# Kernel tuning notes

Measured on AMD Instinct MI355X. Metric: run time of the kernel, lower is better.

The kernel has to match this reference:

```python
import jax, jax.numpy as jnp
import numpy as np
import math

N_ITEMS = 200000
N_USERS = 100000
D = 128
E_II = 3200000
E_UI = 1600000


def spmm(src, dst, val, x, n_rows):
    # out[i] = sum_{e: dst[e]==i} val[e] * x[src[e]]
    return jax.ops.segment_sum(val[:, None] * x[src], dst, num_segments=n_rows)


def leaky_relu(x):
    return jnp.where(x >= 0, x, 0.2 * x)


def setup_inputs() -> dict:
    key = jax.random.key(0)
    ks = jax.random.split(key, 16)
    d = {}
    d["b"] = 2
    d["items_emb"] = jax.random.normal(ks[0], (N_ITEMS, D), dtype=jnp.float32) * 0.1
    for i, rel in enumerate(["p2p_in", "p2p_out", "e2p_in"]):
        d[f"src_{rel}"] = jax.random.randint(ks[1 + 3 * i], (E_II,), 0, N_ITEMS, dtype=jnp.int32)
        d[f"dst_{rel}"] = jax.random.randint(ks[2 + 3 * i], (E_II,), 0, N_ITEMS, dtype=jnp.int32)
        d[f"val_{rel}"] = jax.random.uniform(ks[3 + 3 * i], (E_II,), dtype=jnp.float32) / 16.0
    d["src_ui"] = jax.random.randint(ks[10], (E_UI,), 0, N_ITEMS, dtype=jnp.int32)
    d["dst_ui"] = jax.random.randint(ks[11], (E_UI,), 0, N_USERS, dtype=jnp.int32)
    d["val_ui"] = jax.random.uniform(ks[12], (E_UI,), dtype=jnp.float32) / 16.0
    s = 1.0 / math.sqrt(D)
    d["I_p2p_in"] = jax.random.normal(ks[13], (D, D), dtype=jnp.float32) * s
    d["I_p2p_out"] = jax.random.normal(ks[14], (D, D), dtype=jnp.float32) * s
    d["I_e2p_in"] = jax.random.normal(ks[15], (D, D), dtype=jnp.float32) * s
    return d


def reference(b, items_emb, src_p2p_in, dst_p2p_in, val_p2p_in,
              src_p2p_out, dst_p2p_out, val_p2p_out,
              src_e2p_in, dst_e2p_in, val_e2p_in,
              src_ui, dst_ui, val_ui,
              I_p2p_in, I_p2p_out, I_e2p_in):
    assert b == 2  # static branch, matches torch `if b == 2`
    x = items_emb
    n = x.shape[0]
    inv_sqrt_d = 1.0 / math.sqrt(x.shape[1])

    # multi-relation sparse aggregation (torch.spmm)
    nb_in = spmm(src_p2p_in, dst_p2p_in, val_p2p_in, x, n)
    nb_out = spmm(src_p2p_out, dst_p2p_out, val_p2p_out, x, n)
    nb_e2p = spmm(src_e2p_in, dst_e2p_in, val_e2p_in, x, n)

    # gated attention over relations
    h_in = leaky_relu((x * nb_in) @ I_p2p_in)
    h_out = leaky_relu((x * nb_out) @ I_p2p_out)
    h_e2p = leaky_relu((x * nb_e2p) @ I_e2p_in)
    s_in = jnp.sum(h_in, axis=1) * inv_sqrt_d
    s_out = jnp.sum(h_out, axis=1) * inv_sqrt_d
    s_e2p = jnp.sum(h_e2p, axis=1) * inv_sqrt_d
    score = jax.nn.softmax(jnp.stack((s_in, s_out, s_e2p), axis=1), axis=1)  # [n,3]
    neighbor = (nb_in * score[:, 0:1]
                + nb_out * score[:, 1:2]
                + nb_e2p * score[:, 2:3])

    # uiGNN: user embeddings from item embeddings
    u_emb = spmm(src_ui, dst_ui, val_ui, x, N_USERS)
    return (u_emb, neighbor)
```

## Files before the change

kernel.cpp:

```cpp
#include <hip/hip_runtime.h>

#define D 128
#define N_ITEMS 200000
#define N_USERS 100000
#define TI 32

#define INV_SQRT_D 0.088388347648318447f

__global__ __launch_bounds__(256) void hist_kernel(
    const int* __restrict__ dst, unsigned* __restrict__ counts, int E)
{
    int e = blockIdx.x * 256 + threadIdx.x;
    if (e < E) atomicAdd(&counts[dst[e]], 1u);
}

__global__ __launch_bounds__(256) void scan1_kernel(
    const unsigned* __restrict__ counts, unsigned* __restrict__ offsets,
    unsigned* __restrict__ blocksums, int n)
{
    __shared__ unsigned s[256];
    int tid = threadIdx.x;
    int i = blockIdx.x * 256 + tid;
    unsigned v = (i < n) ? counts[i] : 0u;
    s[tid] = v; __syncthreads();
    #pragma unroll
    for (int off = 1; off < 256; off <<= 1) {
        unsigned t = (tid >= off) ? s[tid - off] : 0u;
        __syncthreads();
        s[tid] += t;
        __syncthreads();
    }
    if (i < n) offsets[i] = s[tid] - v;
    if (tid == 255) blocksums[blockIdx.x] = s[255];
}

__global__ __launch_bounds__(1024) void scan2_kernel(
    unsigned* __restrict__ blocksums, int nb)
{
    __shared__ unsigned s[1024];
    int tid = threadIdx.x;
    unsigned v = (tid < nb) ? blocksums[tid] : 0u;
    s[tid] = v; __syncthreads();
    #pragma unroll
    for (int off = 1; off < 1024; off <<= 1) {
        unsigned t = (tid >= off) ? s[tid - off] : 0u;
        __syncthreads();
        s[tid] += t;
        __syncthreads();
    }
    if (tid < nb) blocksums[tid] = s[tid] - v;
}

__global__ __launch_bounds__(256) void scan3_kernel(
    unsigned* __restrict__ offsets, unsigned* __restrict__ cursor,
    const unsigned* __restrict__ blocksums, int n, unsigned Etot)
{
    int i = blockIdx.x * 256 + threadIdx.x;
    if (i < n) {
        unsigned o = offsets[i] + blocksums[blockIdx.x];
        offsets[i] = o;
        cursor[i] = o;
    }
    if (i == 0) offsets[n] = Etot;
}

__global__ __launch_bounds__(256) void scatter_kernel(
    const int* __restrict__ src, const int* __restrict__ dst,
    const float* __restrict__ val, unsigned* __restrict__ cursor,
    int2* __restrict__ pairs, int E)
{
    int e = blockIdx.x * 256 + threadIdx.x;
    if (e >= E) return;
    unsigned pos = atomicAdd(&cursor[dst[e]], 1u);
    pairs[pos] = make_int2(src[e], __float_as_int(val[e]));
}

__global__ __launch_bounds__(256) void gather_spmm_kernel(
    const unsigned* __restrict__ offsets, const int2* __restrict__ pairs,
    const float4* __restrict__ x4, float4* __restrict__ out4, int nrows)
{
    int row = blockIdx.x * 8 + (threadIdx.x >> 5);
    if (row >= nrows) return;
    int lane = threadIdx.x & 31;
    unsigned j = offsets[row], end = offsets[row + 1];
    float4 acc = make_float4(0.f, 0.f, 0.f, 0.f);
    for (; j + 2 <= end; j += 2) {
        int2 p0 = pairs[j];
        int2 p1 = pairs[j + 1];
        float4 a = x4[(size_t)p0.x * 32 + lane];
        float4 b = x4[(size_t)p1.x * 32 + lane];
        float v0 = __int_as_float(p0.y), v1 = __int_as_float(p1.y);
        acc.x = fmaf(v0, a.x, acc.x); acc.y = fmaf(v0, a.y, acc.y);
        acc.z = fmaf(v0, a.z, acc.z); acc.w = fmaf(v0, a.w, acc.w);
        acc.x = fmaf(v1, b.x, acc.x); acc.y = fmaf(v1, b.y, acc.y);
        acc.z = fmaf(v1, b.z, acc.z); acc.w = fmaf(v1, b.w, acc.w);
    }
    if (j < end) {
        int2 p0 = pairs[j];
        float4 a = x4[(size_t)p0.x * 32 + lane];
        float v0 = __int_as_float(p0.y);
        acc.x = fmaf(v0, a.x, acc.x); acc.y = fmaf(v0, a.y, acc.y);
        acc.z = fmaf(v0, a.z, acc.z); acc.w = fmaf(v0, a.w, acc.w);
    }
    out4[(size_t)row * 32 + lane] = acc;
}

__global__ __launch_bounds__(256) void score_kernel(
    const float* __restrict__ x,
    const float* __restrict__ nb0, const float* __restrict__ nb1,
    const float* __restrict__ nb2,
    const float* __restrict__ I0, const float* __restrict__ I1,
    const float* __restrict__ I2,
    float* __restrict__ w_out)
{
    __shared__ float Ild[D * D];
    __shared__ float Tt[D * 36];
    const int tid = threadIdx.x;
    const int jg = tid & 31;
    const int ig = tid >> 5;
    const int j0 = jg << 2, i0 = ig << 2;
    const int itemBase = blockIdx.x * TI;

    const float* nbs[3] = {nb0, nb1, nb2};
    const float* Is[3]  = {I0, I1, I2};
    float sreg[3][4];

    for (int rel = 0; rel < 3; ++rel) {
        __syncthreads();
        {
            const float4* Ig = (const float4*)Is[rel];
            float4* Il4 = (float4*)Ild;
            #pragma unroll
            for (int t = 0; t < 16; ++t) Il4[tid + t * 256] = Ig[tid + t * 256];
        }
        for (int t = tid; t < TI * D; t += 256) {
            int il = t >> 7;
            int dd = t & 127;
            size_t gi = (size_t)(itemBase + il) * D + dd;
            Tt[dd * 36 + il] = x[gi] * nbs[rel][gi];
        }
        __syncthreads();

        float acc[4][4];
        #pragma unroll
        for (int a = 0; a < 4; ++a)
            #pragma unroll
            for (int b = 0; b < 4; ++b) acc[a][b] = 0.f;

        #pragma unroll 4
        for (int k = 0; k < D; ++k) {
            float4 iv = *(const float4*)&Ild[k * D + j0];
            float4 tv = *(const float4*)&Tt[k * 36 + i0];
            acc[0][0] += tv.x * iv.x; acc[0][1] += tv.x * iv.y;
            acc[0][2] += tv.x * iv.z; acc[0][3] += tv.x * iv.w;
            acc[1][0] += tv.y * iv.x; acc[1][1] += tv.y * iv.y;
            acc[1][2] += tv.y * iv.z; acc[1][3] += tv.y * iv.w;
            acc[2][0] += tv.z * iv.x; acc[2][1] += tv.z * iv.y;
            acc[2][2] += tv.z * iv.z; acc[2][3] += tv.z * iv.w;
            acc[3][0] += tv.w * iv.x; acc[3][1] += tv.w * iv.y;
            acc[3][2] += tv.w * iv.z; acc[3][3] += tv.w * iv.w;
        }

        float ps[4];
        #pragma unroll
        for (int a = 0; a < 4; ++a) {
            float s = 0.f;
            #pragma unroll
            for (int b = 0; b < 4; ++b) {
                float h = acc[a][b];
                s += (h >= 0.f) ? h : 0.2f * h;
            }
            ps[a] = s;
        }
        #pragma unroll
        for (int off = 16; off; off >>= 1) {
            #pragma unroll
            for (int a = 0; a < 4; ++a)
                ps[a] += __shfl_down(ps[a], off, 32);
        }
        if (jg == 0) {
            #pragma unroll
            for (int a = 0; a < 4; ++a) sreg[rel][a] = ps[a] * INV_SQRT_D;
        }
    }

    if (jg == 0) {
        #pragma unroll
        for (int a = 0; a < 4; ++a) {
            float s0 = sreg[0][a], s1 = sreg[1][a], s2 = sreg[2][a];
            float m = fmaxf(s0, fmaxf(s1, s2));
            float e0 = expf(s0 - m), e1 = expf(s1 - m), e2 = expf(s2 - m);
            float inv = 1.f / (e0 + e1 + e2);
            int item = itemBase + i0 + a;
            w_out[item * 3 + 0] = e0 * inv;
            w_out[item * 3 + 1] = e1 * inv;
            w_out[item * 3 + 2] = e2 * inv;
        }
    }
}

__global__ __launch_bounds__(256) void combine_kernel(
    const float4* __restrict__ nb0, const float4* __restrict__ nb1,
    const float4* __restrict__ nb2, const float* __restrict__ w,
    float4* __restrict__ out)
{
    int idx = blockIdx.x * 256 + threadIdx.x;
    if (idx >= N_ITEMS * 32) return;
    int item = idx >> 5;
    float w0 = w[item * 3 + 0], w1 = w[item * 3 + 1], w2 = w[item * 3 + 2];
    float4 a = nb0[idx], b = nb1[idx], c = nb2[idx];
    float4 r;
    r.x = a.x * w0 + b.x * w1 + c.x * w2;
    r.y = a.y * w0 + b.y * w1 + c.y * w2;
    r.z = a.z * w0 + b.z * w1 + c.z * w2;
    r.w = a.w * w0 + b.w * w1 + c.w * w2;
    out[idx] = r;
}

extern "C" void kernel_launch(void* const* d_in, const int* in_sizes, int n_in,
                              void* d_out, int out_size, void* d_ws, size_t ws_size,
                              hipStream_t stream) {
    const float* x       = (const float*)d_in[1];
    const int*   src0    = (const int*)d_in[2];
    const int*   dst0    = (const int*)d_in[3];
    const float* val0    = (const float*)d_in[4];
    const int*   src1    = (const int*)d_in[5];
    const int*   dst1    = (const int*)d_in[6];
    const float* val1    = (const float*)d_in[7];
    const int*   src2    = (const int*)d_in[8];
    const int*   dst2    = (const int*)d_in[9];
    const float* val2    = (const float*)d_in[10];
    const int*   src_ui  = (const int*)d_in[11];
    const int*   dst_ui  = (const int*)d_in[12];
    const float* val_ui  = (const float*)d_in[13];
    const float* I0      = (const float*)d_in[14];
    const float* I1      = (const float*)d_in[15];
    const float* I2      = (const float*)d_in[16];

    const int E_ii = in_sizes[2];
    const int E_ui = in_sizes[11];

    float* u_emb = (float*)d_out;
    float* nb0   = (float*)d_out + (size_t)N_USERS * D;

    float*    nb1       = (float*)d_ws;
    float*    nb2       = nb1 + (size_t)N_ITEMS * D;
    float*    w         = nb2 + (size_t)N_ITEMS * D;
    unsigned* cc        = (unsigned*)(w + (size_t)N_ITEMS * 3);
    unsigned* offsets   = cc + N_ITEMS;
    unsigned* blocksums = offsets + N_ITEMS + 1;
    uintptr_t pu        = ((uintptr_t)(blocksums + 1024) + 15) & ~(uintptr_t)15;
    int2*     pairs_ui  = (int2*)pu;
    int2*     pairs_ii  = (int2*)d_out;

    auto build_and_gather = [&](const int* src, const int* dst, const float* val,
                                int E, int nrows, int2* pairs, float* out) {
        hipMemsetAsync(cc, 0, (size_t)nrows * sizeof(unsigned), stream);
        int gE = (E + 255) / 256;
        int gN = (nrows + 255) / 256;
        hist_kernel<<<gE, 256, 0, stream>>>(dst, cc, E);
        scan1_kernel<<<gN, 256, 0, stream>>>(cc, offsets, blocksums, nrows);
        scan2_kernel<<<1, 1024, 0, stream>>>(blocksums, gN);
        scan3_kernel<<<gN, 256, 0, stream>>>(offsets, cc, blocksums, nrows, (unsigned)E);
        scatter_kernel<<<gE, 256, 0, stream>>>(src, dst, val, cc, pairs, E);
        gather_spmm_kernel<<<(nrows + 7) / 8, 256, 0, stream>>>(
            offsets, pairs, (const float4*)x, (float4*)out, nrows);
    };

    build_and_gather(src0, dst0, val0, E_ii, N_ITEMS, pairs_ii, nb0);
    build_and_gather(src1, dst1, val1, E_ii, N_ITEMS, pairs_ii, nb1);
    build_and_gather(src2, dst2, val2, E_ii, N_ITEMS, pairs_ii, nb2);

    score_kernel<<<N_ITEMS / TI, 256, 0, stream>>>(x, nb0, nb1, nb2, I0, I1, I2, w);

    combine_kernel<<<(N_ITEMS * 32 + 255) / 256, 256, 0, stream>>>(
        (const float4*)nb0, (const float4*)nb1, (const float4*)nb2, w, (float4*)nb0);

    build_and_gather(src_ui, dst_ui, val_ui, E_ui, N_USERS, pairs_ui, u_emb);
}
```

Baseline: 3.136 ms.

## Fuse score and combine kernels, read weight matrices from global/L2

Merges the attention-score kernel and the weighted-combine kernel into one kernel, so the per-item softmax weights stay in shared memory and the nb tiles are re-read while still cache-hot, not in a separate pass. The item tile grows to 64 with an item-major padded shared layout. The 64KB shared copy of each 128x128 weight matrix is dropped and the weights are streamed from global/L2, cutting shared memory use so more blocks fit per CU (launch bounds 256,4). The cost is more global/L2 traffic for the weight matrices and a larger per-thread register tile (4x8).

```diff
diff --git a/kernel.cpp b/kernel.cpp
--- a/kernel.cpp
+++ b/kernel.cpp
@@ -3,7 +3,8 @@
 #define D 128
 #define N_ITEMS 200000
 #define N_USERS 100000
-#define TI 32
+#define TI 64
+#define ST 132
 
 #define INV_SQRT_D 0.088388347648318447f
 
@@ -105,82 +106,105 @@
     out4[(size_t)row * 32 + lane] = acc;
 }
 
-__global__ __launch_bounds__(256) void score_kernel(
-    const float* __restrict__ x,
-    const float* __restrict__ nb0, const float* __restrict__ nb1,
-    const float* __restrict__ nb2,
-    const float* __restrict__ I0, const float* __restrict__ I1,
-    const float* __restrict__ I2,
-    float* __restrict__ w_out)
-{
-    __shared__ float Ild[D * D];
-    __shared__ float Tt[D * 36];
+__global__ __launch_bounds__(256, 4) void score_combine_kernel(
+    const float4* __restrict__ x4,
+    float4* __restrict__ nb0,
+    const float4* __restrict__ nb1, const float4* __restrict__ nb2,
+    const float4* __restrict__ I0, const float4* __restrict__ I1,
+    const float4* __restrict__ I2)
+{
+    __shared__ __align__(16) float Tt[TI * ST];
+    __shared__ float Wl[TI * 3];
     const int tid = threadIdx.x;
-    const int jg = tid & 31;
-    const int ig = tid >> 5;
-    const int j0 = jg << 2, i0 = ig << 2;
+    const int jg = tid & 15;
+    const int ig = tid >> 4;
+    const int i0 = ig << 2;
     const int itemBase = blockIdx.x * TI;
 
-    const float* nbs[3] = {nb0, nb1, nb2};
-    const float* Is[3]  = {I0, I1, I2};
+    const float4* nbs[3] = {(const float4*)nb0, nb1, nb2};
+    const float4* Is[3]  = {I0, I1, I2};
     float sreg[3][4];
 
+    #pragma unroll
     for (int rel = 0; rel < 3; ++rel) {
         __syncthreads();
-        {
-            const float4* Ig = (const float4*)Is[rel];
-            float4* Il4 = (float4*)Ild;
-            #pragma unroll
-            for (int t = 0; t < 16; ++t) Il4[tid + t * 256] = Ig[tid + t * 256];
+        const float4* nbp = nbs[rel];
+        #pragma unroll
+        for (int it = 0; it < 8; ++it) {
+            int f4 = it * 256 + tid;
+            int il = f4 >> 5, dd4 = f4 & 31;
+            size_t g = (size_t)(itemBase + il) * 32 + dd4;
+            float4 a = x4[g], b = nbp[g];
+            float4 p;
+            p.x = a.x * b.x; p.y = a.y * b.y;
+            p.z = a.z * b.z; p.w = a.w * b.w;
+            *(float4*)&Tt[il * ST + (dd4 << 2)] = p;
         }
-        for (int t = tid; t < TI * D; t += 256) {
-            int il = t >> 7;
-            int dd = t & 127;
-            size_t gi = (size_t)(itemBase + il) * D + dd;
-            Tt[dd * 36 + il] = x[gi] * nbs[rel][gi];
-        }
-        __syncthreads();
-
-        float acc[4][4];
+        __syncthreads();
+
+        const float4* Ip = Is[rel];
+        float acc[4][8];
         #pragma unroll
         for (int a = 0; a < 4; ++a)
             #pragma unroll
-            for (int b = 0; b < 4; ++b) acc[a][b] = 0.f;
+            for (int b = 0; b < 8; ++b) acc[a][b] = 0.f;
+
+        const float* t0 = &Tt[(i0 + 0) * ST];
+        const float* t1 = &Tt[(i0 + 1) * ST];
+        const float* t2 = &Tt[(i0 + 2) * ST];
+        const float* t3 = &Tt[(i0 + 3) * ST];
 
         #pragma unroll 4
         for (int k = 0; k < D; ++k) {
-            float4 iv = *(const float4*)&Ild[k * D + j0];
-            float4 tv = *(const float4*)&Tt[k * 36 + i0];
-            acc[0][0] += tv.x * iv.x; acc[0][1] += tv.x * iv.y;
-            acc[0][2] += tv.x * iv.z; acc[0][3] += tv.x * iv.w;
-            acc[1][0] += tv.y * iv.x; acc[1][1] += tv.y * iv.y;
-            acc[1][2] += tv.y * iv.z; acc[1][3] += tv.y * iv.w;
-            acc[2][0] += tv.z * iv.x; acc[2][1] += tv.z * iv.y;
-            acc[2][2] += tv.z * iv.z; acc[2][3] += tv.z * iv.w;
-            acc[3][0] += tv.w * iv.x; acc[3][1] += tv.w * iv.y;
-            acc[3][2] += tv.w * iv.z; acc[3][3] += tv.w * iv.w;
+            float4 iv0 = Ip[k * 32 + (jg << 1)];
+            float4 iv1 = Ip[k * 32 + (jg << 1) + 1];
+            float tv0 = t0[k], tv1 = t1[k], tv2 = t2[k], tv3 = t3[k];
+            acc[0][0] = fmaf(tv0, iv0.x, acc[0][0]);
+            acc[0][1] = fmaf(tv0, iv0.y, acc[0][1]);
+            acc[0][2] = fmaf(tv0, iv0.z, acc[0][2]);
+            acc[0][3] = fmaf(tv0, iv0.w, acc[0][3]);
+            acc[0][4] = fmaf(tv0, iv1.x, acc[0][4]);
+            acc[0][5] = fmaf(tv0, iv1.y, acc[0][5]);
+            acc[0][6] = fmaf(tv0, iv1.z, acc[0][6]);
+            acc[0][7] = fmaf(tv0, iv1.w, acc[0][7]);
+            acc[1][0] = fmaf(tv1, iv0.x, acc[1][0]);
+            acc[1][1] = fmaf(tv1, iv0.y, acc[1][1]);
+            acc[1][2] = fmaf(tv1, iv0.z, acc[1][2]);
+            acc[1][3] = fmaf(tv1, iv0.w, acc[1][3]);
+            acc[1][4] = fmaf(tv1, iv1.x, acc[1][4]);
+            acc[1][5] = fmaf(tv1, iv1.y, acc[1][5]);
+            acc[1][6] = fmaf(tv1, iv1.z, acc[1][6]);
+            acc[1][7] = fmaf(tv1, iv1.w, acc[1][7]);
+            acc[2][0] = fmaf(tv2, iv0.x, acc[2][0]);
+            acc[2][1] = fmaf(tv2, iv0.y, acc[2][1]);
+            acc[2][2] = fmaf(tv2, iv0.z, acc[2][2]);
+            acc[2][3] = fmaf(tv2, iv0.w, acc[2][3]);
+            acc[2][4] = fmaf(tv2, iv1.x, acc[2][4]);
+            acc[2][5] = fmaf(tv2, iv1.y, acc[2][5]);
+            acc[2][6] = fmaf(tv2, iv1.z, acc[2][6]);
+            acc[2][7] = fmaf(tv2, iv1.w, acc[2][7]);
+            acc[3][0] = fmaf(tv3, iv0.x, acc[3][0]);
+            acc[3][1] = fmaf(tv3, iv0.y, acc[3][1]);
+            acc[3][2] = fmaf(tv3, iv0.z, acc[3][2]);
+            acc[3][3] = fmaf(tv3, iv0.w, acc[3][3]);
+            acc[3][4] = fmaf(tv3, iv1.x, acc[3][4]);
+            acc[3][5] = fmaf(tv3, iv1.y, acc[3][5]);
+            acc[3][6] = fmaf(tv3, iv1.z, acc[3][6]);
+            acc[3][7] = fmaf(tv3, iv1.w, acc[3][7]);
         }
 
-        float ps[4];
         #pragma unroll
         for (int a = 0; a < 4; ++a) {
             float s = 0.f;
             #pragma unroll
-            for (int b = 0; b < 4; ++b) {
+            for (int b = 0; b < 8; ++b) {
                 float h = acc[a][b];
                 s += (h >= 0.f) ? h : 0.2f * h;
             }
-            ps[a] = s;
-        }
-        #pragma unroll
-        for (int off = 16; off; off >>= 1) {
             #pragma unroll
-            for (int a = 0; a < 4; ++a)
-                ps[a] += __shfl_down(ps[a], off, 32);
-        }
-        if (jg == 0) {
-            #pragma unroll
-            for (int a = 0; a < 4; ++a) sreg[rel][a] = ps[a] * INV_SQRT_D;
+            for (int off = 8; off; off >>= 1)
+                s += __shfl_down(s, off, 16);
+            sreg[rel][a] = s * INV_SQRT_D;
         }
     }
 
@@ -191,30 +215,28 @@
             float m = fmaxf(s0, fmaxf(s1, s2));
             float e0 = expf(s0 - m), e1 = expf(s1 - m), e2 = expf(s2 - m);
             float inv = 1.f / (e0 + e1 + e2);
-            int item = itemBase + i0 + a;
-            w_out[item * 3 + 0] = e0 * inv;
-            w_out[item * 3 + 1] = e1 * inv;
-            w_out[item * 3 + 2] = e2 * inv;
+            int il = i0 + a;
+            Wl[il * 3 + 0] = e0 * inv;
+            Wl[il * 3 + 1] = e1 * inv;
+            Wl[il * 3 + 2] = e2 * inv;
         }
     }
-}
-
-__global__ __launch_bounds__(256) void combine_kernel(
-    const float4* __restrict__ nb0, const float4* __restrict__ nb1,
-    const float4* __restrict__ nb2, const float* __restrict__ w,
-    float4* __restrict__ out)
-{
-    int idx = blockIdx.x * 256 + threadIdx.x;
-    if (idx >= N_ITEMS * 32) return;
-    int item = idx >> 5;
-    float w0 = w[item * 3 + 0], w1 = w[item * 3 + 1], w2 = w[item * 3 + 2];
-    float4 a = nb0[idx], b = nb1[idx], c = nb2[idx];
-    float4 r;
-    r.x = a.x * w0 + b.x * w1 + c.x * w2;
-    r.y = a.y * w0 + b.y * w1 + c.y * w2;
-    r.z = a.z * w0 + b.z * w1 + c.z * w2;
-    r.w = a.w * w0 + b.w * w1 + c.w * w2;
-    out[idx] = r;
+    __syncthreads();
+
+    #pragma unroll
+    for (int it = 0; it < 8; ++it) {
+        int f4 = it * 256 + tid;
+        int il = f4 >> 5, dd4 = f4 & 31;
+        size_t g = (size_t)(itemBase + il) * 32 + dd4;
+        float w0 = Wl[il * 3 + 0], w1 = Wl[il * 3 + 1], w2 = Wl[il * 3 + 2];
+        float4 a = nb0[g], b = nb1[g], c = nb2[g];
+        float4 r;
+        r.x = fmaf(w0, a.x, fmaf(w1, b.x, w2 * c.x));
+        r.y = fmaf(w0, a.y, fmaf(w1, b.y, w2 * c.y));
+        r.z = fmaf(w0, a.z, fmaf(w1, b.z, w2 * c.z));
+        r.w = fmaf(w0, a.w, fmaf(w1, b.w, w2 * c.w));
+        nb0[g] = r;
+    }
 }
 
 extern "C" void kernel_launch(void* const* d_in, const int* in_sizes, int n_in,
@@ -245,8 +267,7 @@
 
     float*    nb1       = (float*)d_ws;
     float*    nb2       = nb1 + (size_t)N_ITEMS * D;
-    float*    w         = nb2 + (size_t)N_ITEMS * D;
-    unsigned* cc        = (unsigned*)(w + (size_t)N_ITEMS * 3);
+    unsigned* cc        = (unsigned*)(nb2 + (size_t)N_ITEMS * D);
     unsigned* offsets   = cc + N_ITEMS;
     unsigned* blocksums = offsets + N_ITEMS + 1;
     uintptr_t pu        = ((uintptr_t)(blocksums + 1024) + 15) & ~(uintptr_t)15;
@@ -271,10 +292,9 @@
     build_and_gather(src1, dst1, val1, E_ii, N_ITEMS, pairs_ii, nb1);
     build_and_gather(src2, dst2, val2, E_ii, N_ITEMS, pairs_ii, nb2);
 
-    score_kernel<<<N_ITEMS / TI, 256, 0, stream>>>(x, nb0, nb1, nb2, I0, I1, I2, w);
-
-    combine_kernel<<<(N_ITEMS * 32 + 255) / 256, 256, 0, stream>>>(
-        (const float4*)nb0, (const float4*)nb1, (const float4*)nb2, w, (float4*)nb0);
+    score_combine_kernel<<<N_ITEMS / TI, 256, 0, stream>>>(
+        (const float4*)x, (float4*)nb0, (const float4*)nb1, (const float4*)nb2,
+        (const float4*)I0, (const float4*)I1, (const float4*)I2);
 
     build_and_gather(src_ui, dst_ui, val_ui, E_ui, N_USERS, pairs_ui, u_emb);
 }
```

After: 2.889 ms. 1.09x faster.
